# Kernel optimization log

Measured on AMD Instinct MI355X. Metric: run time of the kernel, lower is better.

## Reference

```python
import jax, jax.numpy as jnp
import numpy as np

B, V, L, C, H = 2, 8, 256, 1024, 16

def setup_inputs() -> dict:
    key = jax.random.key(0)
    ks = jax.random.split(key, 6)
    s = 0.02  # init scale for weights
    x = jax.random.normal(ks[0], (B, V, L, C), jnp.float32)
    Wq = jax.random.normal(ks[1], (C, C), jnp.float32) * s
    Wk = jax.random.normal(ks[2], (C, C), jnp.float32) * s
    Wv = jax.random.normal(ks[3], (C, C), jnp.float32) * s
    Wp = jax.random.normal(ks[4], (C, C), jnp.float32) * s
    bp = jnp.zeros((C,), jnp.float32)
    return {"x": x, "Wq": Wq, "Wk": Wk, "Wv": Wv, "Wp": Wp, "bp": bp}

def _view_mask(V, L):
    # view-level allow mask, expanded to token level [S, S]
    vi = jnp.arange(V)
    qv, kv = vi[:, None], vi[None, :]
    cross = ((qv == 0) & (kv == 1)) | ((qv == 1) & (kv == 0))
    later = (qv > 1) | (kv > 1)
    allow = cross | (later & (qv >= kv))  # [V, V]
    return jnp.repeat(jnp.repeat(allow, L, axis=0), L, axis=1)  # [V*L, V*L]

def reference(x, Wq, Wk, Wv, Wp, bp):
    b, v, l, c = x.shape
    h = H
    dh = c // h
    scale = dh ** -0.5
    s = v * l
    xf = x.reshape(b, s, c)
    # torch Linear: y = x @ W.T
    q = (xf @ Wq.T).reshape(b, s, h, dh).transpose(0, 2, 1, 3)  # [b,h,s,dh]
    k = (xf @ Wk.T).reshape(b, s, h, dh).transpose(0, 2, 1, 3)
    vv = (xf @ Wv.T).reshape(b, s, h, dh).transpose(0, 2, 1, 3)
    scores = jnp.einsum('bhqd,bhkd->bhqk', q, k) * scale  # [b,h,s,s]
    mask = _view_mask(v, l)
    scores = jnp.where(mask, scores, -jnp.inf)
    attn = jax.nn.softmax(scores, axis=-1)
    out = jnp.einsum('bhqk,bhkd->bhqd', attn, vv)
    out = out.transpose(0, 2, 1, 3).reshape(b, v, l, c)
    return out @ Wp.T + bp
```

## Files before the change

### kernel.cpp

```cpp
#include <hip/hip_runtime.h>
#include <stdint.h>

typedef unsigned short ushort_t;
typedef __attribute__((ext_vector_type(8))) __bf16 bf16x8;
typedef __attribute__((ext_vector_type(4))) float floatx4;

__device__ __forceinline__ ushort_t f2bf(float f) {
    uint32_t u = __builtin_bit_cast(uint32_t, f);
    u += 0x7fffu + ((u >> 16) & 1u);
    return (ushort_t)(u >> 16);
}

typedef __attribute__((address_space(1))) const void glb_void;
typedef __attribute__((address_space(3))) void lds_void;
__device__ __forceinline__ void gld16(const void* g, void* l) {
    __builtin_amdgcn_global_load_lds((glb_void*)g, (lds_void*)l, 16, 0, 0);
}

#define QSCALE 0.18033688011112042f

__global__ void cast_kernel(const float* __restrict__ x,
                            const float* __restrict__ Wq, const float* __restrict__ Wk,
                            const float* __restrict__ Wv, const float* __restrict__ Wp,
                            ushort_t* __restrict__ xb, ushort_t* __restrict__ Wqkvb,
                            ushort_t* __restrict__ Wpb)
{
    const int64_t NX = 4194304, NW = 1048576;
    int64_t i4 = ((int64_t)blockIdx.x * blockDim.x + threadIdx.x) * 4;
    const float* src; ushort_t* dst; int64_t off;
    if (i4 < NX)            { src = x;  dst = xb;          off = i4; }
    else if (i4 < NX+NW)    { src = Wq; dst = Wqkvb;       off = i4 - NX; }
    else if (i4 < NX+2*NW)  { src = Wk; dst = Wqkvb + NW;  off = i4 - NX - NW; }
    else if (i4 < NX+3*NW)  { src = Wv; dst = Wqkvb + 2*NW;off = i4 - NX - 2*NW; }
    else                    { src = Wp; dst = Wpb;         off = i4 - NX - 3*NW; }
    float4 v = *(const float4*)(src + off);
    ushort4 o;
    o.x = f2bf(v.x); o.y = f2bf(v.y); o.z = f2bf(v.z); o.w = f2bf(v.w);
    *(ushort4*)(dst + off) = o;
}

#define BM 128
#define BK 32

template<int BN_, int MODE>
__global__ __launch_bounds__(256, 3)
void gemm_bt(const ushort_t* __restrict__ A, const ushort_t* __restrict__ Bmat,
             int M, int N, int K,
             ushort_t* __restrict__ qb, ushort_t* __restrict__ kb, ushort_t* __restrict__ vtb,
             float* __restrict__ outf, const float* __restrict__ bias)
{
    constexpr int NB_B = BN_ * BK / 512;
    constexpr int NT   = BN_ / 32;
    constexpr int PER_W = (8 + NB_B) / 4;
    __shared__ ushort_t As[BM * BK];
    __shared__ ushort_t Bs[BN_ * BK];
    const int tid  = threadIdx.x;
    const int lane = tid & 63;
    const int wave = tid >> 6;
    const int m0 = blockIdx.x * BM;
    const int n0 = blockIdx.y * BN_;
    const int wrow = (wave >> 1) * 64;
    const int wcol = (wave & 1) * (BN_ / 2);
    const int q_ = lane >> 4;
    const int ml = lane & 15;

    floatx4 acc[4][NT];
    for (int i = 0; i < 4; i++) for (int j = 0; j < NT; j++) acc[i][j] = floatx4{0.f,0.f,0.f,0.f};

    const int row_l = lane >> 2;
    const int col_l = (lane & 3) * 8;
    const ushort_t* gptr[PER_W]; ushort_t* lptr[PER_W];
    for (int i = 0; i < PER_W; i++) {
        int id = wave * PER_W + i;
        if (id < 8) {
            gptr[i] = A + (int64_t)(m0 + id*16 + row_l) * K + col_l;
            lptr[i] = As + id * 512;
        } else {
            int j = id - 8;
            gptr[i] = Bmat + (int64_t)(n0 + j*16 + row_l) * K + col_l;
            lptr[i] = Bs + j * 512;
        }
    }

    for (int k0 = 0; k0 < K; k0 += BK) {
        __syncthreads();
        for (int i = 0; i < PER_W; i++) gld16(gptr[i] + k0, lptr[i]);
        __syncthreads();
        bf16x8 af[4], bf[NT];
        for (int mt = 0; mt < 4; mt++)
            af[mt] = *(const bf16x8*)(As + (wrow + mt*16 + ml) * BK + q_*8);
        for (int nt = 0; nt < NT; nt++)
            bf[nt] = *(const bf16x8*)(Bs + (wcol + nt*16 + ml) * BK + q_*8);
        for (int mt = 0; mt < 4; mt++)
            for (int nt = 0; nt < NT; nt++)
                acc[mt][nt] = __builtin_amdgcn_mfma_f32_16x16x32_bf16(af[mt], bf[nt], acc[mt][nt], 0, 0, 0);
    }

    if constexpr (MODE == 0) {
        for (int mt = 0; mt < 4; mt++) for (int nt = 0; nt < NT; nt++) {
            floatx4 v = acc[mt][nt];
            int col = n0 + wcol + nt*16 + ml;
            int which = col >> 10;
            int nn = col & 1023;
            int h = nn >> 6, d = nn & 63;
            if (which < 2) {
                ushort_t* dst = (which == 0) ? qb : kb;
                float sc = (which == 0) ? QSCALE : 1.0f;
                for (int r = 0; r < 4; r++) {
                    int rowg = m0 + wrow + mt*16 + q_*4 + r;
                    int b = rowg >> 11, s = rowg & 2047;
                    dst[(((int64_t)(b*16 + h) * 2048 + s) << 6) + d] = f2bf(v[r] * sc);
                }
            } else {
                int rowg0 = m0 + wrow + mt*16 + q_*4;
                int b = rowg0 >> 11, sbase = rowg0 & 2047;
                ushort4 o;
                o.x = f2bf(v[0]); o.y = f2bf(v[1]); o.z = f2bf(v[2]); o.w = f2bf(v[3]);
                *(ushort4*)(vtb + (((int64_t)(b*16 + h) * 64 + d) << 11) + sbase) = o;
            }
        }
    } else {
        for (int mt = 0; mt < 4; mt++) for (int nt = 0; nt < NT; nt++) {
            floatx4 v = acc[mt][nt];
            int col = n0 + wcol + nt*16 + ml;
            float bv = bias[col];
            for (int r = 0; r < 4; r++) {
                int rowg = m0 + wrow + mt*16 + q_*4 + r;
                outf[(int64_t)rowg * N + col] = v[r] + bv;
            }
        }
    }
}

__global__ __launch_bounds__(256, 2)
void attn_kernel(const ushort_t* __restrict__ Q, const ushort_t* __restrict__ Kb,
                 const ushort_t* __restrict__ Vt, ushort_t* __restrict__ Out)
{
    __shared__ ushort_t Kl[8192];
    __shared__ ushort_t Vl[8192];
    __shared__ ushort_t Pl[4 * 4096];

    int bi = blockIdx.x;
    int xcd = bi & 7;
    int sl  = bi >> 3;
    int bh  = xcd + 8 * (sl & 3);
    int rest = sl >> 2;
    int qv = 7 - (rest >> 1);
    int qt = rest & 1;
    int b = bh >> 4, h = bh & 15;
    int tid = threadIdx.x;
    int wave = tid >> 6, lane = tid & 63;
    int q_ = lane >> 4, ml = lane & 15;
    int rlane = lane & 15, clane = lane >> 4;
    int s0 = qv*256 + qt*128 + wave*32;

    const ushort_t* Kbh = Kb + ((int64_t)bh << 17);
    const ushort_t* Vbh = Vt + ((int64_t)bh << 17);
    ushort_t* Pw = Pl + wave * 4096;

    bf16x8 aq0[2], aq1[2];
    for (int qf = 0; qf < 2; qf++) {
        const ushort_t* Qp = Q + (((int64_t)bh*2048 + s0 + qf*16 + ml) << 6) + q_*8;
        aq0[qf] = *(const bf16x8*)(Qp);
        aq1[qf] = *(const bf16x8*)(Qp + 32);
    }

    floatx4 o_acc[2][4];
    for (int qf = 0; qf < 2; qf++) for (int i = 0; i < 4; i++) o_acc[qf][i] = floatx4{0.f,0.f,0.f,0.f};
    float lsum[2][4];
    for (int qf = 0; qf < 2; qf++) for (int r = 0; r < 4; r++) lsum[qf][r] = 0.f;

    int views[8]; int nviews;
    if      (qv == 0) { views[0] = 1; nviews = 1; }
    else if (qv == 1) { views[0] = 0; nviews = 1; }
    else { nviews = qv + 1; for (int i = 0; i < nviews; i++) views[i] = i; }

    for (int vi = 0; vi < nviews; vi++) {
        int kb0 = views[vi] * 256;
        for (int ck = 0; ck < 2; ck++) {
            int koff = kb0 + ck * 128;

            __syncthreads();
            for (int i = 0; i < 8; i++) {
                int id = wave*8 + i;
                if (id < 16) {
                    const ushort_t* gk = Kbh + (((int64_t)(koff + (id >> 1)*16 + rlane)) << 6)
                                             + (id & 1)*32 + clane*8;
                    gld16(gk, Kl + id*512);
                } else {
                    int id2 = id - 16;
                    const ushort_t* gv = Vbh + ((int64_t)((id2 & 3)*16 + rlane) << 11)
                                             + koff + (id2 >> 2)*32 + clane*8;
                    gld16(gv, Vl + id2*512);
                }
            }
            __syncthreads();

            floatx4 sc[2][8];
            for (int kt = 0; kt < 8; kt++) {
                bf16x8 k0 = *(const bf16x8*)(Kl + kt*1024 + lane*8);
                bf16x8 k1 = *(const bf16x8*)(Kl + kt*1024 + 512 + lane*8);
                for (int qf = 0; qf < 2; qf++) {
                    floatx4 cz = floatx4{0.f,0.f,0.f,0.f};
                    cz = __builtin_amdgcn_mfma_f32_16x16x32_bf16(aq0[qf], k0, cz, 0, 0, 0);
                    cz = __builtin_amdgcn_mfma_f32_16x16x32_bf16(aq1[qf], k1, cz, 0, 0, 0);
                    sc[qf][kt] = cz;
                }
            }

            for (int qf = 0; qf < 2; qf++)
                for (int kt = 0; kt < 8; kt++)
                    for (int r = 0; r < 4; r++) {
                        float p = __builtin_amdgcn_exp2f(sc[qf][kt][r]);
                        lsum[qf][r] += p;
                        Pw[qf*2048 + kt*256 + (q_*4 + r)*16 + ml] = f2bf(p);
                    }

            asm volatile("s_waitcnt lgkmcnt(0)" ::: "memory");

            for (int g = 0; g < 4; g++) {
                bf16x8 ap[2];
                for (int qf = 0; qf < 2; qf++)
                    ap[qf] = *(const bf16x8*)(Pw + qf*2048 + (2*g + (q_ >> 1))*256
                                              + ml*16 + (q_ & 1)*8);
                for (int dt = 0; dt < 4; dt++) {
                    bf16x8 vv = *(const bf16x8*)(Vl + (g*4 + dt)*512 + lane*8);
                    for (int qf = 0; qf < 2; qf++)
                        o_acc[qf][dt] = __builtin_amdgcn_mfma_f32_16x16x32_bf16(ap[qf], vv, o_acc[qf][dt], 0, 0, 0);
                }
            }
        }
    }

    for (int off = 1; off < 16; off <<= 1)
        for (int qf = 0; qf < 2; qf++)
            for (int r = 0; r < 4; r++)
                lsum[qf][r] += __shfl_xor(lsum[qf][r], off);

    for (int qf = 0; qf < 2; qf++)
        for (int dt = 0; dt < 4; dt++)
            for (int r = 0; r < 4; r++) {
                float v = o_acc[qf][dt][r] / lsum[qf][r];
                int sr = s0 + qf*16 + q_*4 + r;
                Out[((int64_t)b*2048 + sr) * 1024 + h*64 + dt*16 + ml] = f2bf(v);
            }
}

extern "C" void kernel_launch(void* const* d_in, const int* in_sizes, int n_in,
                              void* d_out, int out_size, void* d_ws, size_t ws_size,
                              hipStream_t stream) {
    const float* x  = (const float*)d_in[0];
    const float* Wq = (const float*)d_in[1];
    const float* Wk = (const float*)d_in[2];
    const float* Wv = (const float*)d_in[3];
    const float* Wp = (const float*)d_in[4];
    const float* bp = (const float*)d_in[5];
    float* out = (float*)d_out;

    char* ws = (char*)d_ws;
    ushort_t* xb    = (ushort_t*)(ws);
    ushort_t* Wqkvb = (ushort_t*)(ws + ((size_t)8  << 20));
    ushort_t* Wpb   = (ushort_t*)(ws + ((size_t)14 << 20));
    ushort_t* qb    = (ushort_t*)(ws + ((size_t)16 << 20));
    ushort_t* kbuf  = (ushort_t*)(ws + ((size_t)24 << 20));
    ushort_t* vtb   = (ushort_t*)(ws + ((size_t)40 << 20));
    ushort_t* attno = xb;

    cast_kernel<<<8192, 256, 0, stream>>>(x, Wq, Wk, Wv, Wp, xb, Wqkvb, Wpb);

    dim3 g0(4096 / BM, 3072 / 128);
    gemm_bt<128, 0><<<g0, 256, 0, stream>>>(xb, Wqkvb, 4096, 3072, 1024,
                                            qb, kbuf, vtb, nullptr, nullptr);

    attn_kernel<<<512, 256, 0, stream>>>(qb, kbuf, vtb, attno);

    dim3 g1(4096 / BM, 1024 / 64);
    gemm_bt<64, 1><<<g1, 256, 0, stream>>>(attno, Wpb, 4096, 1024, 1024,
                                           nullptr, nullptr, nullptr, out, bp);
}
```

Baseline: 186.8 us.

## Load attention K/V straight from global memory with single-wave blocks

Attention blocks shrink from four waves to one wave, and the grid grows to 2048 blocks. K and V tiles are now read directly from global memory into registers instead of being staged through shared memory with block barriers. The per-wave P buffer is padded, with a row stride of 136, to reduce LDS bank conflicts. This removes the LDS staging and the __syncthreads cost, but each wave re-reads K/V from cache with no sharing across waves. The output projection GEMM also switches its N tile from 64 to 128.

```diff
diff --git a/kernel.cpp b/kernel.cpp
--- a/kernel.cpp
+++ b/kernel.cpp
@@ -132,31 +132,26 @@
     }
 }
 
-__global__ __launch_bounds__(256, 2)
+__global__ __launch_bounds__(64)
 void attn_kernel(const ushort_t* __restrict__ Q, const ushort_t* __restrict__ Kb,
                  const ushort_t* __restrict__ Vt, ushort_t* __restrict__ Out)
 {
-    __shared__ ushort_t Kl[8192];
-    __shared__ ushort_t Vl[8192];
-    __shared__ ushort_t Pl[4 * 4096];
+    __shared__ ushort_t Pl[2 * 16 * 136];
 
     int bi = blockIdx.x;
     int xcd = bi & 7;
     int sl  = bi >> 3;
     int bh  = xcd + 8 * (sl & 3);
     int rest = sl >> 2;
-    int qv = 7 - (rest >> 1);
-    int qt = rest & 1;
+    int qv = 7 - (rest >> 3);
+    int qt = rest & 7;
     int b = bh >> 4, h = bh & 15;
-    int tid = threadIdx.x;
-    int wave = tid >> 6, lane = tid & 63;
+    int lane = threadIdx.x & 63;
     int q_ = lane >> 4, ml = lane & 15;
-    int rlane = lane & 15, clane = lane >> 4;
-    int s0 = qv*256 + qt*128 + wave*32;
+    int s0 = qv*256 + qt*32;
 
     const ushort_t* Kbh = Kb + ((int64_t)bh << 17);
     const ushort_t* Vbh = Vt + ((int64_t)bh << 17);
-    ushort_t* Pw = Pl + wave * 4096;
 
     bf16x8 aq0[2], aq1[2];
     for (int qf = 0; qf < 2; qf++) {
@@ -180,26 +175,11 @@
         for (int ck = 0; ck < 2; ck++) {
             int koff = kb0 + ck * 128;
 
-            __syncthreads();
-            for (int i = 0; i < 8; i++) {
-                int id = wave*8 + i;
-                if (id < 16) {
-                    const ushort_t* gk = Kbh + (((int64_t)(koff + (id >> 1)*16 + rlane)) << 6)
-                                             + (id & 1)*32 + clane*8;
-                    gld16(gk, Kl + id*512);
-                } else {
-                    int id2 = id - 16;
-                    const ushort_t* gv = Vbh + ((int64_t)((id2 & 3)*16 + rlane) << 11)
-                                             + koff + (id2 >> 2)*32 + clane*8;
-                    gld16(gv, Vl + id2*512);
-                }
-            }
-            __syncthreads();
-
             floatx4 sc[2][8];
             for (int kt = 0; kt < 8; kt++) {
-                bf16x8 k0 = *(const bf16x8*)(Kl + kt*1024 + lane*8);
-                bf16x8 k1 = *(const bf16x8*)(Kl + kt*1024 + 512 + lane*8);
+                const ushort_t* Kp = Kbh + (((int64_t)(koff + kt*16 + ml)) << 6) + q_*8;
+                bf16x8 k0 = *(const bf16x8*)(Kp);
+                bf16x8 k1 = *(const bf16x8*)(Kp + 32);
                 for (int qf = 0; qf < 2; qf++) {
                     floatx4 cz = floatx4{0.f,0.f,0.f,0.f};
                     cz = __builtin_amdgcn_mfma_f32_16x16x32_bf16(aq0[qf], k0, cz, 0, 0, 0);
@@ -213,7 +193,7 @@
                     for (int r = 0; r < 4; r++) {
                         float p = __builtin_amdgcn_exp2f(sc[qf][kt][r]);
                         lsum[qf][r] += p;
-                        Pw[qf*2048 + kt*256 + (q_*4 + r)*16 + ml] = f2bf(p);
+                        Pl[qf*2176 + (q_*4 + r)*136 + kt*16 + ml] = f2bf(p);
                     }
 
             asm volatile("s_waitcnt lgkmcnt(0)" ::: "memory");
@@ -221,14 +201,15 @@
             for (int g = 0; g < 4; g++) {
                 bf16x8 ap[2];
                 for (int qf = 0; qf < 2; qf++)
-                    ap[qf] = *(const bf16x8*)(Pw + qf*2048 + (2*g + (q_ >> 1))*256
-                                              + ml*16 + (q_ & 1)*8);
+                    ap[qf] = *(const bf16x8*)(Pl + qf*2176 + ml*136 + g*32 + q_*8);
                 for (int dt = 0; dt < 4; dt++) {
-                    bf16x8 vv = *(const bf16x8*)(Vl + (g*4 + dt)*512 + lane*8);
+                    const ushort_t* Vp = Vbh + ((int64_t)(dt*16 + ml) << 11) + koff + g*32 + q_*8;
+                    bf16x8 vv = *(const bf16x8*)(Vp);
                     for (int qf = 0; qf < 2; qf++)
                         o_acc[qf][dt] = __builtin_amdgcn_mfma_f32_16x16x32_bf16(ap[qf], vv, o_acc[qf][dt], 0, 0, 0);
                 }
             }
+            asm volatile("s_waitcnt lgkmcnt(0)" ::: "memory");
         }
     }
 
@@ -272,9 +253,9 @@
     gemm_bt<128, 0><<<g0, 256, 0, stream>>>(xb, Wqkvb, 4096, 3072, 1024,
                                             qb, kbuf, vtb, nullptr, nullptr);
 
-    attn_kernel<<<512, 256, 0, stream>>>(qb, kbuf, vtb, attno);
-
-    dim3 g1(4096 / BM, 1024 / 64);
-    gemm_bt<64, 1><<<g1, 256, 0, stream>>>(attno, Wpb, 4096, 1024, 1024,
-                                           nullptr, nullptr, nullptr, out, bp);
-}
+    attn_kernel<<<2048, 64, 0, stream>>>(qb, kbuf, vtb, attno);
+
+    dim3 g1(4096 / BM, 1024 / 128);
+    gemm_bt<128, 1><<<g1, 256, 0, stream>>>(attno, Wpb, 4096, 1024, 1024,
+                                            nullptr, nullptr, nullptr, out, bp);
+}
```

Result: slower. 235.0 us (+25.8%).

## Keep attention probabilities in registers via transposed MFMA, halve block size

Applied to the files above, without the earlier changes.

The attention kernel now computes S^T = K·Q^T, so the score accumulator layout matches the B-operand layout of the P·V MFMA. Probabilities are packed into registers directly instead of round-tripping through a per-wave LDS P buffer, and K rows are loaded with a permutation so this works. Blocks shrink to 2 waves with twice as many blocks, and wave 0 loads K while wave 1 loads V. The output store becomes vectorized ushort4 writes. This removes LDS traffic and the LDS footprint for P, but each block now reuses its K/V tiles for fewer query rows.

```diff
diff --git a/kernel.cpp b/kernel.cpp
--- a/kernel.cpp
+++ b/kernel.cpp
@@ -132,118 +132,128 @@
     }
 }
 
-__global__ __launch_bounds__(256, 2)
+__global__ __launch_bounds__(128, 2)
 void attn_kernel(const ushort_t* __restrict__ Q, const ushort_t* __restrict__ Kb,
                  const ushort_t* __restrict__ Vt, ushort_t* __restrict__ Out)
 {
     __shared__ ushort_t Kl[8192];
     __shared__ ushort_t Vl[8192];
-    __shared__ ushort_t Pl[4 * 4096];
 
     int bi = blockIdx.x;
     int xcd = bi & 7;
     int sl  = bi >> 3;
     int bh  = xcd + 8 * (sl & 3);
     int rest = sl >> 2;
-    int qv = 7 - (rest >> 1);
-    int qt = rest & 1;
+    int qv = 7 - (rest >> 2);
+    int qt = rest & 3;
     int b = bh >> 4, h = bh & 15;
     int tid = threadIdx.x;
     int wave = tid >> 6, lane = tid & 63;
     int q_ = lane >> 4, ml = lane & 15;
-    int rlane = lane & 15, clane = lane >> 4;
-    int s0 = qv*256 + qt*128 + wave*32;
+    int s0 = qv*256 + qt*64 + wave*32;
 
     const ushort_t* Kbh = Kb + ((int64_t)bh << 17);
     const ushort_t* Vbh = Vt + ((int64_t)bh << 17);
-    ushort_t* Pw = Pl + wave * 4096;
-
-    bf16x8 aq0[2], aq1[2];
-    for (int qf = 0; qf < 2; qf++) {
-        const ushort_t* Qp = Q + (((int64_t)bh*2048 + s0 + qf*16 + ml) << 6) + q_*8;
-        aq0[qf] = *(const bf16x8*)(Qp);
-        aq1[qf] = *(const bf16x8*)(Qp + 32);
-    }
+
+    bf16x8 bq[2][2];
+    for (int qf = 0; qf < 2; qf++)
+        for (int hh = 0; hh < 2; hh++)
+            bq[qf][hh] = *(const bf16x8*)(Q + (((int64_t)bh*2048 + s0 + qf*16 + ml) << 6)
+                                          + hh*32 + q_*8);
 
     floatx4 o_acc[2][4];
     for (int qf = 0; qf < 2; qf++) for (int i = 0; i < 4; i++) o_acc[qf][i] = floatx4{0.f,0.f,0.f,0.f};
-    float lsum[2][4];
-    for (int qf = 0; qf < 2; qf++) for (int r = 0; r < 4; r++) lsum[qf][r] = 0.f;
+    float lsum[2] = {0.f, 0.f};
 
     int views[8]; int nviews;
     if      (qv == 0) { views[0] = 1; nviews = 1; }
     else if (qv == 1) { views[0] = 0; nviews = 1; }
     else { nviews = qv + 1; for (int i = 0; i < nviews; i++) views[i] = i; }
 
+    int m_ = lane & 15, q5 = lane >> 4;
+    int kperm = (m_ >> 2)*8 + (m_ & 3);
+
     for (int vi = 0; vi < nviews; vi++) {
         int kb0 = views[vi] * 256;
         for (int ck = 0; ck < 2; ck++) {
             int koff = kb0 + ck * 128;
 
             __syncthreads();
-            for (int i = 0; i < 8; i++) {
-                int id = wave*8 + i;
-                if (id < 16) {
-                    const ushort_t* gk = Kbh + (((int64_t)(koff + (id >> 1)*16 + rlane)) << 6)
-                                             + (id & 1)*32 + clane*8;
-                    gld16(gk, Kl + id*512);
-                } else {
-                    int id2 = id - 16;
-                    const ushort_t* gv = Vbh + ((int64_t)((id2 & 3)*16 + rlane) << 11)
-                                             + koff + (id2 >> 2)*32 + clane*8;
-                    gld16(gv, Vl + id2*512);
+            if (wave == 0) {
+                #pragma unroll
+                for (int id = 0; id < 16; id++) {
+                    int w = id >> 2, t = (id >> 1) & 1, hh = id & 1;
+                    const ushort_t* g = Kbh
+                        + (((int64_t)(koff + w*32 + t*4 + kperm)) << 6) + hh*32 + q5*8;
+                    gld16(g, Kl + id*512);
+                }
+            } else {
+                #pragma unroll
+                for (int id = 0; id < 16; id++) {
+                    int w = id >> 2, dt = id & 3;
+                    const ushort_t* g = Vbh
+                        + ((int64_t)(dt*16 + m_) << 11) + koff + w*32 + q5*8;
+                    gld16(g, Vl + id*512);
                 }
             }
             __syncthreads();
 
-            floatx4 sc[2][8];
-            for (int kt = 0; kt < 8; kt++) {
-                bf16x8 k0 = *(const bf16x8*)(Kl + kt*1024 + lane*8);
-                bf16x8 k1 = *(const bf16x8*)(Kl + kt*1024 + 512 + lane*8);
+            #pragma unroll
+            for (int w = 0; w < 4; w++) {
+                floatx4 st[2][2];
+                #pragma unroll
+                for (int t = 0; t < 2; t++) {
+                    bf16x8 k0 = *(const bf16x8*)(Kl + (w*4 + t*2 + 0)*512 + lane*8);
+                    bf16x8 k1 = *(const bf16x8*)(Kl + (w*4 + t*2 + 1)*512 + lane*8);
+                    #pragma unroll
+                    for (int qf = 0; qf < 2; qf++) {
+                        floatx4 cz = floatx4{0.f,0.f,0.f,0.f};
+                        cz = __builtin_amdgcn_mfma_f32_16x16x32_bf16(k0, bq[qf][0], cz, 0, 0, 0);
+                        cz = __builtin_amdgcn_mfma_f32_16x16x32_bf16(k1, bq[qf][1], cz, 0, 0, 0);
+                        st[t][qf] = cz;
+                    }
+                }
+                bf16x8 pb[2];
+                #pragma unroll
                 for (int qf = 0; qf < 2; qf++) {
-                    floatx4 cz = floatx4{0.f,0.f,0.f,0.f};
-                    cz = __builtin_amdgcn_mfma_f32_16x16x32_bf16(aq0[qf], k0, cz, 0, 0, 0);
-                    cz = __builtin_amdgcn_mfma_f32_16x16x32_bf16(aq1[qf], k1, cz, 0, 0, 0);
-                    sc[qf][kt] = cz;
-                }
-            }
-
-            for (int qf = 0; qf < 2; qf++)
-                for (int kt = 0; kt < 8; kt++)
-                    for (int r = 0; r < 4; r++) {
-                        float p = __builtin_amdgcn_exp2f(sc[qf][kt][r]);
-                        lsum[qf][r] += p;
-                        Pw[qf*2048 + kt*256 + (q_*4 + r)*16 + ml] = f2bf(p);
-                    }
-
-            asm volatile("s_waitcnt lgkmcnt(0)" ::: "memory");
-
-            for (int g = 0; g < 4; g++) {
-                bf16x8 ap[2];
-                for (int qf = 0; qf < 2; qf++)
-                    ap[qf] = *(const bf16x8*)(Pw + qf*2048 + (2*g + (q_ >> 1))*256
-                                              + ml*16 + (q_ & 1)*8);
+                    union { ushort_t u[8]; bf16x8 v; } pu;
+                    #pragma unroll
+                    for (int t = 0; t < 2; t++)
+                        #pragma unroll
+                        for (int r = 0; r < 4; r++) {
+                            float p = __builtin_amdgcn_exp2f(st[t][qf][r]);
+                            lsum[qf] += p;
+                            pu.u[t*4 + r] = f2bf(p);
+                        }
+                    pb[qf] = pu.v;
+                }
+                #pragma unroll
                 for (int dt = 0; dt < 4; dt++) {
-                    bf16x8 vv = *(const bf16x8*)(Vl + (g*4 + dt)*512 + lane*8);
+                    bf16x8 vf = *(const bf16x8*)(Vl + (w*4 + dt)*512 + lane*8);
+                    #pragma unroll
                     for (int qf = 0; qf < 2; qf++)
-                        o_acc[qf][dt] = __builtin_amdgcn_mfma_f32_16x16x32_bf16(ap[qf], vv, o_acc[qf][dt], 0, 0, 0);
-                }
-            }
-        }
-    }
-
-    for (int off = 1; off < 16; off <<= 1)
+                        o_acc[qf][dt] = __builtin_amdgcn_mfma_f32_16x16x32_bf16(vf, pb[qf], o_acc[qf][dt], 0, 0, 0);
+                }
+            }
+        }
+    }
+
+    for (int off = 16; off < 64; off <<= 1)
         for (int qf = 0; qf < 2; qf++)
-            for (int r = 0; r < 4; r++)
-                lsum[qf][r] += __shfl_xor(lsum[qf][r], off);
-
-    for (int qf = 0; qf < 2; qf++)
-        for (int dt = 0; dt < 4; dt++)
-            for (int r = 0; r < 4; r++) {
-                float v = o_acc[qf][dt][r] / lsum[qf][r];
-                int sr = s0 + qf*16 + q_*4 + r;
-                Out[((int64_t)b*2048 + sr) * 1024 + h*64 + dt*16 + ml] = f2bf(v);
-            }
+            lsum[qf] += __shfl_xor(lsum[qf], off);
+
+    for (int qf = 0; qf < 2; qf++) {
+        float inv = 1.0f / lsum[qf];
+        int sr = s0 + qf*16 + ml;
+        for (int dt = 0; dt < 4; dt++) {
+            ushort4 o;
+            o.x = f2bf(o_acc[qf][dt][0] * inv);
+            o.y = f2bf(o_acc[qf][dt][1] * inv);
+            o.z = f2bf(o_acc[qf][dt][2] * inv);
+            o.w = f2bf(o_acc[qf][dt][3] * inv);
+            *(ushort4*)(Out + ((int64_t)b*2048 + sr) * 1024 + h*64 + dt*16 + q_*4) = o;
+        }
+    }
 }
 
 extern "C" void kernel_launch(void* const* d_in, const int* in_sizes, int n_in,
@@ -272,7 +282,7 @@
     gemm_bt<128, 0><<<g0, 256, 0, stream>>>(xb, Wqkvb, 4096, 3072, 1024,
                                             qb, kbuf, vtb, nullptr, nullptr);
 
-    attn_kernel<<<512, 256, 0, stream>>>(qb, kbuf, vtb, attno);
+    attn_kernel<<<1024, 128, 0, stream>>>(qb, kbuf, vtb, attno);
 
     dim3 g1(4096 / BM, 1024 / 64);
     gemm_bt<64, 1><<<g1, 256, 0, stream>>>(attno, Wpb, 4096, 1024, 1024,
```

Measured after the change: 186.2 us. Within noise of the previous version (-0.3%).
